# Kernel optimization log

Measured on AMD Instinct MI355X. Metric: run time of the kernel, lower is better.

Reference implementation:

```python
import jax, jax.numpy as jnp
import numpy as np
from jax import lax

BLANK_ID = 0
NEG_INF = -1e10  # finite stand-in for log(0); module uses LOG_0 = -1e10

B, T, H, V, L = 32, 1000, 512, 2048, 100


def setup_inputs() -> dict:
    key = jax.random.key(0)
    k1, k2, k3, k4, k5, k6 = jax.random.split(key, 6)
    eouts = jax.random.normal(k1, (B, T, H), dtype=jnp.float32)
    W = jax.random.normal(k2, (V, H), dtype=jnp.float32) * (1.0 / np.sqrt(H))
    b = jax.random.normal(k3, (V,), dtype=jnp.float32) * 0.01
    ys = jax.random.randint(k4, (B, L), 1, V, dtype=jnp.int32)  # labels exclude blank=0
    ylens = jax.random.randint(k5, (B,), L // 2, L + 1, dtype=jnp.int32)
    # ensure T_b >= 2*L_b + 1 so every alignment is feasible
    elens = jnp.clip(jax.random.randint(k6, (B,), T // 2, T + 1, dtype=jnp.int32), 2 * L + 1, T)
    return {"eouts": eouts, "W": W, "b": b, "ys": ys, "elens": elens, "ylens": ylens}


def ctc_loss_sum(log_probs, ys, elens, ylens):
    """Batched CTC forward DP. log_probs: [B,T,V]; ys: [B,L]; returns sum loss."""
    Bb, Tt, Vv = log_probs.shape
    Ll = ys.shape[1]
    S = 2 * Ll + 1
    # extended label sequence: blank, y1, blank, y2, ..., blank
    ext = jnp.zeros((Bb, S), dtype=jnp.int32).at[:, 1::2].set(ys)
    # gather per-frame log-probs of extended labels: [B,T,S]
    lp_ext = jnp.take_along_axis(log_probs, jnp.broadcast_to(ext[:, None, :], (Bb, Tt, S)), axis=2)
    # s-2 skip allowed iff ext[s] != blank and ext[s] != ext[s-2]
    ext_m2 = jnp.pad(ext, ((0, 0), (2, 0)), constant_values=-1)[:, :S]
    skip_ok = (ext != BLANK_ID) & (ext != ext_m2)
    valid = jnp.arange(S)[None, :] < (2 * ylens[:, None] + 1)  # [B,S]

    a0 = jnp.full((Bb, S), NEG_INF, dtype=log_probs.dtype)
    a0 = a0.at[:, 0].set(lp_ext[:, 0, 0]).at[:, 1].set(lp_ext[:, 0, 1])
    a0 = jnp.where(valid, a0, NEG_INF)

    def step(a, lp_t):  # a: [B,S], lp_t: [B,S]
        a1 = a
        a2 = jnp.pad(a, ((0, 0), (1, 0)), constant_values=NEG_INF)[:, :S]
        a3 = jnp.where(skip_ok, jnp.pad(a, ((0, 0), (2, 0)), constant_values=NEG_INF)[:, :S], NEG_INF)
        new = jnp.logaddexp(jnp.logaddexp(a1, a2), a3) + lp_t
        new = jnp.where(valid, new, NEG_INF)
        return new, new

    _, alphas_rest = lax.scan(step, a0, jnp.swapaxes(lp_ext, 0, 1)[1:])  # [T-1,B,S]
    alphas = jnp.concatenate([a0[None], alphas_rest], axis=0)  # [T,B,S]

    a_final = alphas[elens - 1, jnp.arange(Bb)]  # [B,S]
    last = jnp.take_along_axis(a_final, (2 * ylens)[:, None], axis=1)[:, 0]
    prev = jnp.take_along_axis(a_final, (2 * ylens - 1)[:, None], axis=1)[:, 0]
    loss_b = -jnp.logaddexp(last, prev)
    # zero_infinity=True: replace non-finite (numerically huge) losses with 0
    loss_b = jnp.where(loss_b < -0.5 * NEG_INF, loss_b, 0.0)
    return jnp.sum(loss_b)


def reference(eouts, W, b, ys, elens, ylens):
    logits = jnp.einsum("bth,vh->btv", eouts, W) + b  # self.output(eouts)
    log_probs = jax.nn.log_softmax(logits, axis=-1)
    loss_ctc = ctc_loss_sum(log_probs, ys, elens, ylens) / eouts.shape[0]
    return loss_ctc
```

## Files before the change

### kernel.cpp

```cpp
#include <hip/hip_runtime.h>
#include <hip/hip_bf16.h>

#define B_ 32
#define T_ 1000
#define H_ 512
#define V_ 2048
#define L_ 100
#define M_ (B_*T_)
#define GSTRIDE 104
#define LOG2E 1.4426950408889634f
#define LSE_SHIFT 48.0f
#define BIAS60 1.152921504606847e18f

typedef __attribute__((ext_vector_type(8))) short bf16x8;
typedef __attribute__((ext_vector_type(4))) float f32x4;

#define AS_G(p)  ((const __attribute__((address_space(1))) unsigned int*)(p))
#define AS_L(p)  ((__attribute__((address_space(3))) unsigned int*)(p))

__device__ __forceinline__ unsigned short f2bf(float x) {
    unsigned int u; __builtin_memcpy(&u, &x, 4);
    unsigned int r = (u + 0x7fffu + ((u >> 16) & 1u)) >> 16;
    return (unsigned short)r;
}

__device__ __forceinline__ float dpp_shr1(float x) {
    int r = __builtin_amdgcn_update_dpp(0, __builtin_bit_cast(int, x), 0x138, 0xf, 0xf, false);
    return __builtin_bit_cast(float, r);
}
template<int CTRL>
__device__ __forceinline__ float fmax_dpp(float x) {
    int s = __builtin_amdgcn_update_dpp(0, __builtin_bit_cast(int, x), CTRL, 0xf, 0xf, false);
    return fmaxf(x, __builtin_bit_cast(float, s));
}
__device__ __forceinline__ float wave_max_nonneg(float x) {
    x = fmax_dpp<0x111>(x);
    x = fmax_dpp<0x112>(x);
    x = fmax_dpp<0x114>(x);
    x = fmax_dpp<0x118>(x);
    x = fmax_dpp<0x142>(x);
    x = fmax_dpp<0x143>(x);
    return __builtin_bit_cast(float, __builtin_amdgcn_readlane(__builtin_bit_cast(int, x), 63));
}

__global__ __launch_bounds__(256) void prep_kernel(
        const float* __restrict__ eouts, const float* __restrict__ W,
        unsigned short* __restrict__ eb, unsigned short* __restrict__ wb,
        float* __restrict__ Srow, float* __restrict__ out)
{
    const int E4 = M_*H_/4;
    const int W4 = V_*H_/4;
    const int S4 = M_/4;
    int idx = blockIdx.x*256 + threadIdx.x;
    if (idx == 0) out[0] = 0.f;
    if (idx < E4) {
        float4 v = ((const float4*)eouts)[idx];
        ushort4 o; o.x=f2bf(v.x); o.y=f2bf(v.y); o.z=f2bf(v.z); o.w=f2bf(v.w);
        ((ushort4*)eb)[idx] = o;
    } else if (idx < E4 + W4) {
        int j = idx - E4;
        float4 v = ((const float4*)W)[j];
        ushort4 o; o.x=f2bf(v.x); o.y=f2bf(v.y); o.z=f2bf(v.z); o.w=f2bf(v.w);
        ((ushort4*)wb)[j] = o;
    } else if (idx < E4 + W4 + S4) {
        int j = idx - E4 - W4;
        ((float4*)Srow)[j] = make_float4(0.f,0.f,0.f,0.f);
    }
}

__global__ __launch_bounds__(256) void gemm_lse_kernel(
        const unsigned short* __restrict__ eb, const unsigned short* __restrict__ wb,
        const float* __restrict__ bias, float* __restrict__ Srow)
{
    __shared__ __align__(16) unsigned short As[128*64];
    __shared__ __align__(16) unsigned short Bs[128*64];
    __shared__ float rs[128];
    const int tid  = threadIdx.x;
    const int w    = tid >> 6;
    const int lane = tid & 63;
    const int m    = lane & 15;
    const int q    = lane >> 4;
    const int wrow = w >> 1;
    const int wcol = w & 1;
    const int nbase = blockIdx.x * 128;
    const int mbase = blockIdx.y * 128;
    if (tid < 128) rs[tid] = 0.f;

    const int rbase = w*32 + (lane >> 3);
    const int k8    = (((lane & 7) ^ ((lane >> 3) & 7)) * 8);
    const int rl    = m & 7;

    f32x4 acc[4][4];
    #pragma unroll
    for (int i=0;i<4;i++)
        #pragma unroll
        for (int j=0;j<4;j++) acc[i][j] = (f32x4){0.f,0.f,0.f,0.f};

    for (int kc = 0; kc < 8; ++kc) {
        __syncthreads();
        #pragma unroll
        for (int j = 0; j < 4; ++j) {
            const unsigned short* ga = eb + (size_t)(mbase + rbase + j*8)*H_ + kc*64 + k8;
            __builtin_amdgcn_global_load_lds(AS_G(ga), AS_L(As + (w*4+j)*512), 16, 0, 0);
            const unsigned short* gw = wb + (size_t)(nbase + rbase + j*8)*H_ + kc*64 + k8;
            __builtin_amdgcn_global_load_lds(AS_G(gw), AS_L(Bs + (w*4+j)*512), 16, 0, 0);
        }
        __syncthreads();
        #pragma unroll
        for (int kk = 0; kk < 2; ++kk) {
            const int sw = ((kk*4 + q) ^ rl) * 8;
            bf16x8 af[4], bfr[4];
            #pragma unroll
            for (int mi=0;mi<4;mi++)
                af[mi] = *(const bf16x8*)(As + (wrow*8 + mi*2 + (m>>3))*512 + rl*64 + sw);
            #pragma unroll
            for (int ni=0;ni<4;ni++)
                bfr[ni] = *(const bf16x8*)(Bs + (wcol*8 + ni*2 + (m>>3))*512 + rl*64 + sw);
            #pragma unroll
            for (int mi=0;mi<4;mi++)
                #pragma unroll
                for (int ni=0;ni<4;ni++)
                    acc[mi][ni] = __builtin_amdgcn_mfma_f32_16x16x32_bf16(
                        af[mi], bfr[ni], acc[mi][ni], 0, 0, 0);
        }
    }

    float bv[4];
    #pragma unroll
    for (int ni=0;ni<4;ni++) bv[ni] = bias[nbase + wcol*64 + ni*16 + m];
    #pragma unroll
    for (int mi=0;mi<4;mi++) {
        #pragma unroll
        for (int r=0;r<4;r++) {
            float s = 0.f;
            #pragma unroll
            for (int ni=0;ni<4;ni++)
                s += exp2f((acc[mi][ni][r] + bv[ni]) * LOG2E - LSE_SHIFT);
            s += __shfl_xor(s, 1);
            s += __shfl_xor(s, 2);
            s += __shfl_xor(s, 4);
            s += __shfl_xor(s, 8);
            if (m == 0) atomicAdd(&rs[wrow*64 + mi*16 + q*4 + r], s);
        }
    }
    __syncthreads();
    if (tid < 128) atomicAdd(&Srow[mbase + tid], rs[tid]);
}

__global__ __launch_bounds__(256) void gather_mfma_kernel(
        const unsigned short* __restrict__ eb, const unsigned short* __restrict__ wb,
        const float* __restrict__ bias, const int* __restrict__ ys,
        const float* __restrict__ Srow, float* __restrict__ g)
{
    __shared__ __align__(16) unsigned short As[128*64];
    __shared__ __align__(16) unsigned short Bs[128*64];
    __shared__ float ls[128];
    const int tid  = threadIdx.x;
    const int w    = tid >> 6;
    const int lane = tid & 63;
    const int m    = lane & 15;
    const int q    = lane >> 4;
    const int wrow = w >> 1;
    const int wcol = w & 1;
    const int b    = blockIdx.y;
    const int tb   = blockIdx.x * 128;

    if (tid < 128) {
        int t = tb + tid;
        ls[tid] = (t < T_) ? (LSE_SHIFT + log2f(Srow[b*T_ + t])) : 0.f;
    }

    const int rbase = w*32 + (lane >> 3);
    const int k8    = (((lane & 7) ^ ((lane >> 3) & 7)) * 8);
    const int rl    = m & 7;

    int vrow[4];
    #pragma unroll
    for (int j=0;j<4;++j) {
        int labr = rbase + j*8;
        vrow[j] = (labr == 0 || labr > L_) ? 0 : ys[b*L_ + labr - 1];
    }
    int labc[4]; float bv[4];
    #pragma unroll
    for (int ni=0;ni<4;++ni) {
        int lab = wcol*64 + ni*16 + m;
        labc[ni] = lab;
        int v = (lab == 0 || lab > L_) ? 0 : ys[b*L_ + lab - 1];
        bv[ni] = bias[v];
    }

    f32x4 acc[4][4];
    #pragma unroll
    for (int i=0;i<4;i++)
        #pragma unroll
        for (int j=0;j<4;j++) acc[i][j] = (f32x4){0.f,0.f,0.f,0.f};

    for (int kc = 0; kc < 8; ++kc) {
        __syncthreads();
        #pragma unroll
        for (int j = 0; j < 4; ++j) {
            const unsigned short* ga = eb + (size_t)(b*T_ + tb + rbase + j*8)*H_ + kc*64 + k8;
            __builtin_amdgcn_global_load_lds(AS_G(ga), AS_L(As + (w*4+j)*512), 16, 0, 0);
            const unsigned short* gw = wb + (size_t)vrow[j]*H_ + kc*64 + k8;
            __builtin_amdgcn_global_load_lds(AS_G(gw), AS_L(Bs + (w*4+j)*512), 16, 0, 0);
        }
        __syncthreads();
        #pragma unroll
        for (int kk = 0; kk < 2; ++kk) {
            const int sw = ((kk*4 + q) ^ rl) * 8;
            bf16x8 af[4], bfr[4];
            #pragma unroll
            for (int mi=0;mi<4;mi++)
                af[mi] = *(const bf16x8*)(As + (wrow*8 + mi*2 + (m>>3))*512 + rl*64 + sw);
            #pragma unroll
            for (int ni=0;ni<4;ni++)
                bfr[ni] = *(const bf16x8*)(Bs + (wcol*8 + ni*2 + (m>>3))*512 + rl*64 + sw);
            #pragma unroll
            for (int mi=0;mi<4;mi++)
                #pragma unroll
                for (int ni=0;ni<4;ni++)
                    acc[mi][ni] = __builtin_amdgcn_mfma_f32_16x16x32_bf16(
                        af[mi], bfr[ni], acc[mi][ni], 0, 0, 0);
        }
    }

    #pragma unroll
    for (int mi=0;mi<4;mi++) {
        #pragma unroll
        for (int r=0;r<4;r++) {
            int trow = wrow*64 + mi*16 + q*4 + r;
            int t = tb + trow;
            float l2 = ls[trow];
            #pragma unroll
            for (int ni=0;ni<4;ni++) {
                if (t < T_ && labc[ni] <= L_) {
                    float p = exp2f((acc[mi][ni][r] + bv[ni]) * LOG2E - l2);
                    int off = (labc[ni] == 0) ? 0 : labc[ni] + 1;
                    g[(size_t)(b*T_ + t)*GSTRIDE + off] = p;
                }
            }
        }
    }
}

__global__ __launch_bounds__(128, 1) void ctc_dp_kernel(
        const float* __restrict__ g, const int* __restrict__ ys,
        const int* __restrict__ elens, const int* __restrict__ ylens,
        float* __restrict__ out)
{
    __shared__ __align__(16) float ring[2*2048];
    const int b    = blockIdx.x;
    const int tid  = threadIdx.x;
    const int wv   = tid >> 6;
    const int lane = tid & 63;
    const float* gb = g + (size_t)b * T_ * GSTRIDE;
    const int ylen = ylens[b];
    const int elen = elens[b];
    const int kmax = (elen - 1) >> 4;

    const int Sv   = 2*ylen + 1;
    const int s0   = 4*lane;
    const float msk0 = (s0   < Sv) ? 1.f : 0.f;
    const float msk1 = (s0+1 < Sv) ? 1.f : 0.f;
    const float msk2 = (s0+2 < Sv) ? 1.f : 0.f;
    const float msk3 = (s0+3 < Sv) ? 1.f : 0.f;
    const int l0 = 2*lane, l1 = 2*lane + 1;
    int i0 = min(max(l0,1), L_-1);
    int i1 = min(l1, L_-1);
    const float sk1 = (l0 >= 1 && l0 < L_ && ys[b*L_+i0] != ys[b*L_+i0-1]) ? 1.f : 0.f;
    const float sk3 = (l1 < L_        && ys[b*L_+i1] != ys[b*L_+i1-1]) ? 1.f : 0.f;

    float a0 = 0.f, a1 = 0.f, a2 = 0.f, a3 = 0.f, C2 = 0.f;
    if (wv == 0) {
        a0 = (lane == 0) ? gb[0] : 0.f;
        a1 = (lane == 0) ? gb[2] : 0.f;
    } else {
        #pragma unroll
        for (int s = 0; s < 8; ++s) {
            int srow = min(2*s, T_-2);
            __builtin_amdgcn_global_load_lds(AS_G(gb + (size_t)srow*GSTRIDE + 4*lane),
                                             AS_L(ring + s*256), 16, 0, 0);
        }
    }

    auto dpstep = [&](float p0, float p1, float p2, float p3) {
        float um1 = dpp_shr1(a3);
        float n0 = a0 + um1;
        float n1 = a1 + a0 + sk1*um1;
        float n2 = a2 + a1;
        float n3 = a3 + a2 + sk3*a1;
        a0 = n0*p0; a1 = n1*p1; a2 = n2*p2; a3 = n3*p3;
    };
    auto renorm = [&]() {
        float mm = wave_max_nonneg(fmaxf(fmaxf(a0,a1), fmaxf(a2,a3)));
        if (mm > 0.f) {
            float rr = fminf(__fdividef(BIAS60, mm), 3.0e38f);
            C2 -= __log2f(rr);
            a0 *= rr; a1 *= rr; a2 *= rr; a3 *= rr;
        }
    };

    __syncthreads();

    for (int k = 0; k <= kmax; ++k) {
        if (wv == 1) {
            if (k < kmax) {
                float* dset = ring + ((k+1) & 1)*2048;
                int pbase = 8*(k + 1);
                #pragma unroll
                for (int s = 0; s < 8; ++s) {
                    int srow = min(2*(pbase + s), T_-2);
                    __builtin_amdgcn_global_load_lds(AS_G(gb + (size_t)srow*GSTRIDE + 4*lane),
                                                     AS_L(dset + s*256), 16, 0, 0);
                }
            }
        } else {
            const float* sb = ring + (k & 1)*2048;
            float P0[16], P1[16], P2[16], P3[16];
            #pragma unroll
            for (int s = 0; s < 8; ++s) {
                const float* slot = sb + s*256;
                float pb0 = slot[0];
                float pb1 = slot[104];
                float2 lo = *(const float2*)(slot + 2  + 2*lane);
                float2 hi = *(const float2*)(slot + 106 + 2*lane);
                P0[2*s]   = pb0*msk0; P1[2*s]   = lo.x*msk1;
                P2[2*s]   = pb0*msk2; P3[2*s]   = lo.y*msk3;
                P0[2*s+1] = pb1*msk0; P1[2*s+1] = hi.x*msk1;
                P2[2*s+1] = pb1*msk2; P3[2*s+1] = hi.y*msk3;
            }
            const int t0 = 16*k;
            #pragma unroll
            for (int j = 0; j < 16; ++j) {
                int t = t0 + j;
                if (t > 0 && t < elen)
                    dpstep(P0[j], P1[j], P2[j], P3[j]);
                if ((j & 7) == 7) renorm();
            }
        }
        __syncthreads();
    }

    if (wv == 0) {
        int sA = 2*ylen, sB = sA - 1;
        float vA = __shfl((sA & 2) ? a2 : a0, sA >> 2);
        float vB = __shfl((sB & 2) ? a3 : a1, sB >> 2);
        if (lane == 0) {
            float sum = vA + vB;
            float loss = 0.f;
            if (sum > 0.f) {
                loss = -(log2f(sum) + C2) * 0.6931471805599453f;
                if (!(loss < 5e9f)) loss = 0.f;
            }
            atomicAdd(out, loss * (1.0f/B_));
        }
    }
}

extern "C" void kernel_launch(void* const* d_in, const int* in_sizes, int n_in,
                              void* d_out, int out_size, void* d_ws, size_t ws_size,
                              hipStream_t stream)
{
    const float* eouts = (const float*)d_in[0];
    const float* W     = (const float*)d_in[1];
    const float* bias  = (const float*)d_in[2];
    const int*   ys    = (const int*)d_in[3];
    const int*   elens = (const int*)d_in[4];
    const int*   ylens = (const int*)d_in[5];
    float* out = (float*)d_out;

    char* ws = (char*)d_ws;
    unsigned short* eb = (unsigned short*)ws;
    unsigned short* wb = (unsigned short*)(ws + 32768000);
    float* Srow        = (float*)(ws + 34865152);
    float* g           = (float*)(ws + 34993152);

    prep_kernel<<<17057, 256, 0, stream>>>(eouts, W, eb, wb, Srow, out);
    gemm_lse_kernel<<<dim3(16, 250), 256, 0, stream>>>(eb, wb, bias, Srow);
    gather_mfma_kernel<<<dim3(8, 32), 256, 0, stream>>>(eb, wb, bias, ys, Srow, g);
    ctc_dp_kernel<<<B_, 128, 0, stream>>>(g, ys, elens, ylens, out);
}
```

Measured before the change: 304.8 us.

## Rewrite GEMM-LSE kernel with 256x256 tiles and double-buffered LDS pipeline

The logits GEMM with fused row sum-exp now uses 256x256 output tiles computed by 512 threads (8 waves). It double-buffers LDS with direct global-to-LDS loads that are interleaved with MFMA phases, controlled by explicit vmcnt/lgkmcnt waits, raw barriers and s_setprio around the MFMA bursts. The aim is to hide global load latency behind compute and to cut per-tile global traffic through larger reuse. In exchange, 1000 blocks of 512 threads with 128 KB of LDS allow only one block per CU, and correctness depends on the hand-written wait counts.

```diff
diff --git a/kernel.cpp b/kernel.cpp
--- a/kernel.cpp
+++ b/kernel.cpp
@@ -68,68 +68,135 @@
     }
 }
 
-__global__ __launch_bounds__(256) void gemm_lse_kernel(
+__global__ __launch_bounds__(512, 1) void gemm_lse_kernel(
         const unsigned short* __restrict__ eb, const unsigned short* __restrict__ wb,
         const float* __restrict__ bias, float* __restrict__ Srow)
 {
-    __shared__ __align__(16) unsigned short As[128*64];
-    __shared__ __align__(16) unsigned short Bs[128*64];
-    __shared__ float rs[128];
+    __shared__ __align__(16) unsigned short Ab[2][256*64];
+    __shared__ __align__(16) unsigned short Bb[2][256*64];
+    __shared__ float rs[256];
     const int tid  = threadIdx.x;
     const int w    = tid >> 6;
     const int lane = tid & 63;
     const int m    = lane & 15;
-    const int q    = lane >> 4;
-    const int wrow = w >> 1;
-    const int wcol = w & 1;
-    const int nbase = blockIdx.x * 128;
-    const int mbase = blockIdx.y * 128;
-    if (tid < 128) rs[tid] = 0.f;
-
-    const int rbase = w*32 + (lane >> 3);
-    const int k8    = (((lane & 7) ^ ((lane >> 3) & 7)) * 8);
-    const int rl    = m & 7;
-
-    f32x4 acc[4][4];
-    #pragma unroll
-    for (int i=0;i<4;i++)
+    const int qh   = lane >> 4;
+    const int wr   = w >> 2;
+    const int wc   = w & 3;
+    const int rl   = m & 7;
+    const int lrow = lane >> 3;
+    const int k8   = ((lane & 7) ^ lrow) * 8;
+    const int nbase = blockIdx.x * 256;
+    const int mbase = blockIdx.y * 256;
+
+    if (tid < 256) rs[tid] = 0.f;
+
+    f32x4 acc[8][4];
+    #pragma unroll
+    for (int i=0;i<8;i++)
         #pragma unroll
         for (int j=0;j<4;j++) acc[i][j] = (f32x4){0.f,0.f,0.f,0.f};
-
-    for (int kc = 0; kc < 8; ++kc) {
-        __syncthreads();
-        #pragma unroll
-        for (int j = 0; j < 4; ++j) {
-            const unsigned short* ga = eb + (size_t)(mbase + rbase + j*8)*H_ + kc*64 + k8;
-            __builtin_amdgcn_global_load_lds(AS_G(ga), AS_L(As + (w*4+j)*512), 16, 0, 0);
-            const unsigned short* gw = wb + (size_t)(nbase + rbase + j*8)*H_ + kc*64 + k8;
-            __builtin_amdgcn_global_load_lds(AS_G(gw), AS_L(Bs + (w*4+j)*512), 16, 0, 0);
-        }
-        __syncthreads();
-        #pragma unroll
-        for (int kk = 0; kk < 2; ++kk) {
-            const int sw = ((kk*4 + q) ^ rl) * 8;
-            bf16x8 af[4], bfr[4];
-            #pragma unroll
-            for (int mi=0;mi<4;mi++)
-                af[mi] = *(const bf16x8*)(As + (wrow*8 + mi*2 + (m>>3))*512 + rl*64 + sw);
-            #pragma unroll
-            for (int ni=0;ni<4;ni++)
-                bfr[ni] = *(const bf16x8*)(Bs + (wcol*8 + ni*2 + (m>>3))*512 + rl*64 + sw);
-            #pragma unroll
-            for (int mi=0;mi<4;mi++)
-                #pragma unroll
-                for (int ni=0;ni<4;ni++)
-                    acc[mi][ni] = __builtin_amdgcn_mfma_f32_16x16x32_bf16(
-                        af[mi], bfr[ni], acc[mi][ni], 0, 0, 0);
-        }
+    bf16x8 af[2][2], bfr[4][2];
+
+#define STAGE_A(sel, r, kt) do { \
+        const unsigned short* _s = eb + (size_t)(mbase + (r)*64 + w*8 + lrow)*H_ + (kt)*64 + k8; \
+        __builtin_amdgcn_global_load_lds(AS_G(_s), AS_L(&Ab[sel][((r)*64 + w*8)*64]), 16, 0, 0); \
+    } while(0)
+#define STAGE_B(sel, r, kt) do { \
+        const unsigned short* _s = wb + (size_t)(nbase + (r)*64 + w*8 + lrow)*H_ + (kt)*64 + k8; \
+        __builtin_amdgcn_global_load_lds(AS_G(_s), AS_L(&Bb[sel][((r)*64 + w*8)*64]), 16, 0, 0); \
+    } while(0)
+
+#define LOADB(sel) \
+    _Pragma("unroll") \
+    for (int ni=0; ni<4; ++ni) { \
+        const int brow = wc*64 + ni*16 + m; \
+        bfr[ni][0] = *(const bf16x8*)(&Bb[sel][brow*64 + ((qh ^ rl))*8]); \
+        bfr[ni][1] = *(const bf16x8*)(&Bb[sel][brow*64 + (((4+qh) ^ rl))*8]); \
+    }
+#define LOADA(sel, qq) \
+    _Pragma("unroll") \
+    for (int mi2=0; mi2<2; ++mi2) { \
+        const int arow = wr*128 + ((qq)*2+mi2)*16 + m; \
+        af[mi2][0] = *(const bf16x8*)(&Ab[sel][arow*64 + ((qh ^ rl))*8]); \
+        af[mi2][1] = *(const bf16x8*)(&Ab[sel][arow*64 + (((4+qh) ^ rl))*8]); \
+    }
+#define MFMA16(qq) \
+    __builtin_amdgcn_s_setprio(1); \
+    _Pragma("unroll") \
+    for (int mi2=0; mi2<2; ++mi2) \
+        _Pragma("unroll") \
+        for (int ni=0; ni<4; ++ni) { \
+            acc[(qq)*2+mi2][ni] = __builtin_amdgcn_mfma_f32_16x16x32_bf16(af[mi2][0], bfr[ni][0], acc[(qq)*2+mi2][ni], 0, 0, 0); \
+            acc[(qq)*2+mi2][ni] = __builtin_amdgcn_mfma_f32_16x16x32_bf16(af[mi2][1], bfr[ni][1], acc[(qq)*2+mi2][ni], 0, 0, 0); \
+        } \
+    __builtin_amdgcn_s_setprio(0);
+#define BARX() __builtin_amdgcn_s_barrier()
+#define WAIT_LGKM() asm volatile("s_waitcnt lgkmcnt(0)" ::: "memory")
+
+    STAGE_B(0,0,0); STAGE_B(0,1,0);
+    STAGE_B(0,2,0); STAGE_B(0,3,0);
+    STAGE_A(0,1,0); STAGE_A(0,3,0);
+    STAGE_A(0,0,0); STAGE_A(0,2,0);
+    STAGE_B(1,0,1); STAGE_B(1,1,1);
+    STAGE_B(1,2,1); STAGE_B(1,3,1);
+    STAGE_A(1,1,1); STAGE_A(1,3,1);
+    asm volatile("s_waitcnt vmcnt(6)" ::: "memory");
+    BARX();
+
+    for (int it = 0; it < 4; ++it) {
+        const int kt1 = 2*it + 1, kt2 = 2*it + 2, kt3 = 2*it + 3;
+        const bool st = (it < 3);
+        LOADB(0) LOADA(0,3)
+        STAGE_A(1,0,kt1); STAGE_A(1,2,kt1);
+        BARX(); WAIT_LGKM();
+        MFMA16(3)
+        BARX();
+        LOADA(0,2)
+        if (st) { STAGE_B(0,0,kt2); STAGE_B(0,1,kt2); }
+        BARX(); WAIT_LGKM();
+        MFMA16(2)
+        BARX();
+        LOADA(0,1)
+        if (st) { STAGE_B(0,2,kt2); STAGE_B(0,3,kt2); }
+        BARX(); WAIT_LGKM();
+        MFMA16(1)
+        BARX();
+        LOADA(0,0)
+        if (st) { STAGE_A(0,1,kt2); STAGE_A(0,3,kt2); }
+        BARX(); WAIT_LGKM();
+        MFMA16(0)
+        if (st) { asm volatile("s_waitcnt vmcnt(6)" ::: "memory"); }
+        else    { asm volatile("s_waitcnt vmcnt(0)" ::: "memory"); }
+        BARX();
+        LOADB(1) LOADA(1,3)
+        if (st) { STAGE_A(0,0,kt2); STAGE_A(0,2,kt2); }
+        BARX(); WAIT_LGKM();
+        MFMA16(3)
+        BARX();
+        LOADA(1,2)
+        if (st) { STAGE_B(1,0,kt3); STAGE_B(1,1,kt3); }
+        BARX(); WAIT_LGKM();
+        MFMA16(2)
+        BARX();
+        LOADA(1,1)
+        if (st) { STAGE_B(1,2,kt3); STAGE_B(1,3,kt3); }
+        BARX(); WAIT_LGKM();
+        MFMA16(1)
+        BARX();
+        LOADA(1,0)
+        if (st) { STAGE_A(1,1,kt3); STAGE_A(1,3,kt3); }
+        BARX(); WAIT_LGKM();
+        MFMA16(0)
+        if (st) { asm volatile("s_waitcnt vmcnt(6)" ::: "memory"); }
+        else    { asm volatile("s_waitcnt vmcnt(0)" ::: "memory"); }
+        BARX();
     }
 
     float bv[4];
     #pragma unroll
-    for (int ni=0;ni<4;ni++) bv[ni] = bias[nbase + wcol*64 + ni*16 + m];
-    #pragma unroll
-    for (int mi=0;mi<4;mi++) {
+    for (int ni=0;ni<4;ni++) bv[ni] = bias[nbase + wc*64 + ni*16 + m];
+    #pragma unroll
+    for (int mi=0;mi<8;mi++) {
         #pragma unroll
         for (int r=0;r<4;r++) {
             float s = 0.f;
@@ -140,11 +207,18 @@
             s += __shfl_xor(s, 2);
             s += __shfl_xor(s, 4);
             s += __shfl_xor(s, 8);
-            if (m == 0) atomicAdd(&rs[wrow*64 + mi*16 + q*4 + r], s);
+            if (m == 0) atomicAdd(&rs[wr*128 + mi*16 + qh*4 + r], s);
         }
     }
     __syncthreads();
-    if (tid < 128) atomicAdd(&Srow[mbase + tid], rs[tid]);
+    if (tid < 256) atomicAdd(&Srow[mbase + tid], rs[tid]);
+#undef STAGE_A
+#undef STAGE_B
+#undef LOADB
+#undef LOADA
+#undef MFMA16
+#undef BARX
+#undef WAIT_LGKM
 }
 
 __global__ __launch_bounds__(256) void gather_mfma_kernel(
@@ -376,7 +450,7 @@
     float* g           = (float*)(ws + 34993152);
 
     prep_kernel<<<17057, 256, 0, stream>>>(eouts, W, eb, wb, Srow, out);
-    gemm_lse_kernel<<<dim3(16, 250), 256, 0, stream>>>(eb, wb, bias, Srow);
+    gemm_lse_kernel<<<dim3(8, 125), 512, 0, stream>>>(eb, wb, bias, Srow);
     gather_mfma_kernel<<<dim3(8, 32), 256, 0, stream>>>(eb, wb, bias, ys, Srow, g);
     ctc_dp_kernel<<<B_, 128, 0, stream>>>(g, ys, elens, ylens, out);
 }
```

New measurement: 281.7 us. 1.08x faster.
